# Optimization experiments

Hardware: AMD Instinct MI355X
Metric: run time of the kernel (lower is better)

Reference implementation:

```python
import jax, jax.numpy as jnp
import numpy as np

NH = 8            # num_heads
LN_EPS = 1e-5


def _alibi_slopes(n):
    # n is a power of two here (8)
    start = 2.0 ** (-2.0 ** (-(np.log2(n) - 3)))
    return np.array([start * (start ** i) for i in range(n)], dtype=np.float32)


def _ln(x, w, b):
    m = x.mean(-1, keepdims=True)
    v = ((x - m) ** 2).mean(-1, keepdims=True)
    return (x - m) / jnp.sqrt(v + LN_EPS) * w + b


def setup_inputs() -> dict:
    key = jax.random.key(0)
    B, S, D_in, H, L = 2, 2048, 192, 512, 4
    ks = jax.random.split(key, 8)
    p = lambda k, shape: 0.02 * jax.random.normal(k, shape, dtype=jnp.float32)
    return {
        "x": jax.random.normal(ks[0], (B, S, D_in), dtype=jnp.float32),
        "w_emb": p(ks[1], (H, D_in)), "b_emb": jnp.zeros((H,), jnp.float32),
        "ln1_w": jnp.ones((L, H), jnp.float32), "ln1_b": jnp.zeros((L, H), jnp.float32),
        "inp_w": p(ks[2], (L, 3 * H, H)), "inp_b": jnp.zeros((L, 3 * H), jnp.float32),
        "outp_w": p(ks[3], (L, H, H)), "outp_b": jnp.zeros((L, H), jnp.float32),
        "ln2_w": jnp.ones((L, H), jnp.float32), "ln2_b": jnp.zeros((L, H), jnp.float32),
        "w1": p(ks[4], (L, 4 * H, H)), "b1": jnp.zeros((L, 4 * H), jnp.float32),
        "w2": p(ks[5], (L, H, 4 * H)), "b2": jnp.zeros((L, H), jnp.float32),
        "fln_w": jnp.ones((H,), jnp.float32), "fln_b": jnp.zeros((H,), jnp.float32),
        "w_out": p(ks[6], (D_in, H)), "b_out": jnp.zeros((D_in,), jnp.float32),
    }


def reference(x, w_emb, b_emb, ln1_w, ln1_b, inp_w, inp_b, outp_w, outp_b,
              ln2_w, ln2_b, w1, b1, w2, b2, fln_w, fln_b, w_out, b_out):
    B, S, _ = x.shape
    H = w_emb.shape[0]
    L = ln1_w.shape[0]
    hd = H // NH
    scale = 1.0 / np.sqrt(hd)

    h = x @ w_emb.T + b_emb                                   # [B,S,H]

    # ALiBi + causal additive mask, shared across batch: [NH,S,S]
    slopes = jnp.asarray(_alibi_slopes(NH))
    pos = jnp.arange(S)
    rel = pos[:, None] - pos[None, :]                         # i - j
    causal = jnp.where(rel < 0, -jnp.inf, 0.0).astype(jnp.float32)
    mask = -slopes[:, None, None] * jnp.maximum(rel, 0).astype(jnp.float32) + causal

    for l in range(L):
        xn = _ln(h, ln1_w[l], ln1_b[l])
        qkv = xn @ inp_w[l].T + inp_b[l]                      # [B,S,3H]
        q, k, v = jnp.split(qkv, 3, axis=-1)
        q = q.reshape(B, S, NH, hd)
        k = k.reshape(B, S, NH, hd)
        v = v.reshape(B, S, NH, hd)
        scores = jnp.einsum('bqhd,bkhd->bhqk', q, k) * scale + mask[None]
        attn = jax.nn.softmax(scores, axis=-1)
        o = jnp.einsum('bhqk,bkhd->bqhd', attn, v).reshape(B, S, H)
        h = h + o @ outp_w[l].T + outp_b[l]
        xn2 = _ln(h, ln2_w[l], ln2_b[l])
        mlp = jax.nn.gelu(xn2 @ w1[l].T + b1[l], approximate=False) @ w2[l].T + b2[l]
        h = h + mlp

    h = _ln(h, fln_w, fln_b)
    return h @ w_out.T + b_out
```

## Files before the change

### kernel.cpp

```cpp
#include <hip/hip_runtime.h>
#include <hip/hip_bf16.h>
#include <math.h>

typedef short v8s __attribute__((ext_vector_type(8)));
typedef float v4f __attribute__((ext_vector_type(4)));
typedef unsigned int v2u __attribute__((ext_vector_type(2)));
typedef __hip_bfloat16 bf16;

#define LDQK 1056
#define LDVT 2080

__device__ inline short f2b(float f){
  __hip_bfloat16 h = __float2bfloat16(f);
  return __builtin_bit_cast(short, h);
}
__device__ inline unsigned int pack2t(float x, float y){
  unsigned int xb = __builtin_bit_cast(unsigned int, x);
  unsigned int yb = __builtin_bit_cast(unsigned int, y);
  return (xb >> 16) | (yb & 0xFFFF0000u);
}
__device__ inline v4f v4f_zero(){ v4f z = {0.f,0.f,0.f,0.f}; return z; }

__device__ inline void gload_lds16(const void* g, void* l){
  __builtin_amdgcn_global_load_lds(
      (__attribute__((address_space(1))) void*)(g),
      (__attribute__((address_space(3))) void*)(l), 16, 0, 0);
}

struct CvtSeg { const float* s; bf16* d; int n4; };
struct CvtArgs { CvtSeg seg[7]; };

__global__ __launch_bounds__(256) void k_cvt7(CvtArgs a){
  const CvtSeg sg = a.seg[blockIdx.y];
  int i = blockIdx.x*256 + threadIdx.x;
  const int stride = gridDim.x*256;
  for (; i < sg.n4; i += stride){
    float4 v = ((const float4*)sg.s)[i];
    short4 o;
    o.x = f2b(v.x); o.y = f2b(v.y); o.z = f2b(v.z); o.w = f2b(v.w);
    ((short4*)sg.d)[i] = o;
  }
}

__global__ __launch_bounds__(256) void k_ln(const float* __restrict__ x,
                                            const float* __restrict__ w,
                                            const float* __restrict__ b,
                                            bf16* __restrict__ out){
  const int row  = blockIdx.x*4 + (threadIdx.x>>6);
  const int lane = threadIdx.x & 63;
  const float* xr = x + (size_t)row*512 + lane*8;
  float4 a = *(const float4*)xr;
  float4 c = *(const float4*)(xr+4);
  float s  = a.x+a.y+a.z+a.w + c.x+c.y+c.z+c.w;
  float sq = a.x*a.x+a.y*a.y+a.z*a.z+a.w*a.w + c.x*c.x+c.y*c.y+c.z*c.z+c.w*c.w;
  #pragma unroll
  for (int m=1;m<64;m<<=1){ s += __shfl_xor(s,m); sq += __shfl_xor(sq,m); }
  const float mean = s*(1.f/512.f);
  const float rstd = rsqrtf(sq*(1.f/512.f) - mean*mean + 1e-5f);
  const float* wp = w + lane*8; const float* bp = b + lane*8;
  float4 w0 = *(const float4*)wp, w1v = *(const float4*)(wp+4);
  float4 b0 = *(const float4*)bp, b1v = *(const float4*)(bp+4);
  v8s o;
  o[0]=f2b((a.x-mean)*rstd*w0.x +b0.x);
  o[1]=f2b((a.y-mean)*rstd*w0.y +b0.y);
  o[2]=f2b((a.z-mean)*rstd*w0.z +b0.z);
  o[3]=f2b((a.w-mean)*rstd*w0.w +b0.w);
  o[4]=f2b((c.x-mean)*rstd*w1v.x+b1v.x);
  o[5]=f2b((c.y-mean)*rstd*w1v.y+b1v.y);
  o[6]=f2b((c.z-mean)*rstd*w1v.z+b1v.z);
  o[7]=f2b((c.w-mean)*rstd*w1v.w+b1v.w);
  *(v8s*)(out + (size_t)row*512 + lane*8) = o;
}

enum { EPI_F32=0, EPI_BF16=1, EPI_F32RES=2, EPI_GELU=3, EPI_VT=4, EPI_QKV=5 };

template<int BM, int BN, int BK, int WR, int EPI>
__global__ __launch_bounds__(256) void k_gemm(
    const bf16* __restrict__ A, const bf16* __restrict__ W,
    const float* __restrict__ bias,
    float* __restrict__ resf, bf16* __restrict__ outb,
    const int M, const int N, const int K, const int ldo)
{
  constexpr int WC = 4/WR;
  constexpr int FM = BM/(WR*16);
  constexpr int FN = BN/(WC*16);
  constexpr int KK = BK/32;
  constexpr int CPR = BK/8;
  __shared__ __align__(16) bf16 As[2][BM*BK];
  __shared__ __align__(16) bf16 Bs[2][BN*BK];
  const int tid  = threadIdx.x;
  const int wave = tid>>6, lane = tid&63;
  const int r = lane&15, g = lane>>4;
  const int bm = blockIdx.x*BM, bn = blockIdx.y*BN;
  const int wr = (WR==1) ? 0 : (wave>>1);
  const int wc = (WR==1) ? wave : (wave&1);

  v4f acc[FM][FN];
  #pragma unroll
  for (int i=0;i<FM;++i)
    #pragma unroll
    for (int j=0;j<FN;++j) acc[i][j] = v4f_zero();

  const int NT = K / BK;

  auto stage = [&](int buf, int kb){
    constexpr int ACH = BM*CPR;
    #pragma unroll
    for (int it=0; it<(ACH+255)/256; ++it){
      const int cb = it*256 + wave*64;
      if ((ACH & 255) == 0 || cb < ACH){
        const int cc = cb + lane;
        const bf16* gp = A + (size_t)(bm + cc/CPR)*K + kb + (cc%CPR)*8;
        gload_lds16(gp, &As[buf][cc*8]);
      }
    }
    constexpr int BCH = BN*CPR;
    #pragma unroll
    for (int it=0; it<(BCH+255)/256; ++it){
      const int cb = it*256 + wave*64;
      if ((BCH & 255) == 0 || cb < BCH){
        const int cc = cb + lane;
        const bf16* gp = W + (size_t)(bn + cc/CPR)*K + kb + (cc%CPR)*8;
        gload_lds16(gp, &Bs[buf][cc*8]);
      }
    }
  };

  stage(0, 0);
  int cur = 0;
  for (int t=0; t<NT; ++t){
    __syncthreads();
    if (t+1 < NT) stage(cur^1, (t+1)*BK);
    const bf16* ap = &As[cur][(wr*(BM/WR) + r)*BK + g*8];
    const bf16* bp = &Bs[cur][(wc*(BN/WC) + r)*BK + g*8];
    #pragma unroll
    for (int kk=0; kk<KK; ++kk){
      v8s af[FM], bfr[FN];
      #pragma unroll
      for (int i=0;i<FM;++i) af[i] = *(const v8s*)(ap + i*16*BK + kk*32);
      #pragma unroll
      for (int j=0;j<FN;++j) bfr[j] = *(const v8s*)(bp + j*16*BK + kk*32);
      #pragma unroll
      for (int i=0;i<FM;++i)
        #pragma unroll
        for (int j=0;j<FN;++j)
          acc[i][j] = __builtin_amdgcn_mfma_f32_16x16x32_bf16(af[i], bfr[j], acc[i][j], 0,0,0);
    }
    cur ^= 1;
  }

  #pragma unroll
  for (int j=0;j<FN;++j){
    const int col = bn + wc*(BN/WC) + j*16 + r;
    const float bv = bias[col];
    #pragma unroll
    for (int i=0;i<FM;++i){
      const int row0 = bm + wr*(BM/WR) + i*16 + g*4;
      if constexpr (EPI==EPI_QKV){
        if (col < 1024){
          #pragma unroll
          for (int q=0;q<4;++q)
            outb[(size_t)(row0+q)*LDQK + col] = __float2bfloat16(acc[i][j][q] + bv);
        } else {
          const int d = col - 1024;
          bf16* vt = (bf16*)resf
                   + (((size_t)(row0>>11)*8 + (d>>6))*64 + (d&63))*(size_t)LDVT + (row0&2047);
          short4 st;
          st.x = f2b(acc[i][j][0] + bv);
          st.y = f2b(acc[i][j][1] + bv);
          st.z = f2b(acc[i][j][2] + bv);
          st.w = f2b(acc[i][j][3] + bv);
          *(short4*)vt = st;
        }
      } else if constexpr (EPI==EPI_VT){
        bf16* vt = outb + (((size_t)(row0>>11)*8 + (col>>6))*64 + (col&63))*(size_t)ldo + (row0&2047);
        short4 st;
        st.x = f2b(acc[i][j][0] + bv);
        st.y = f2b(acc[i][j][1] + bv);
        st.z = f2b(acc[i][j][2] + bv);
        st.w = f2b(acc[i][j][3] + bv);
        *(short4*)vt = st;
      } else {
        #pragma unroll
        for (int q=0;q<4;++q){
          float v = acc[i][j][q] + bv;
          const size_t idx = (size_t)(row0+q)*ldo + col;
          if constexpr (EPI==EPI_F32)         resf[idx] = v;
          else if constexpr (EPI==EPI_F32RES) resf[idx] += v;
          else if constexpr (EPI==EPI_BF16)   outb[idx] = __float2bfloat16(v);
          else if constexpr (EPI==EPI_GELU){
            float gv = 0.5f*v*(1.f + erff(v*0.70710678118654752f));
            outb[idx] = __float2bfloat16(gv);
          }
        }
      }
    }
  }
}

__global__ __launch_bounds__(256) void k_attn(const bf16* __restrict__ qk,
                                              const bf16* __restrict__ vt,
                                              bf16* __restrict__ o){
  const int flat  = blockIdx.x;
  const int qi    = flat >> 4;
  const int head  = flat & 7;
  const int batch = (flat >> 3) & 1;
  const int sp = threadIdx.x>>6, lane = threadIdx.x&63;
  const int r = lane&15, g = lane>>4;
  const float LOG2E = 1.4426950408889634f;
  const float scale2 = 0.125f * LOG2E;
  const float slope2 = exp2f(-(float)(head+1)) * LOG2E;
  const bf16* qbase = qk + (size_t)batch*2048*LDQK + head*64;
  const bf16* kbase = qbase + 512;
  const bf16* vbase = vt + (size_t)(batch*8 + head)*64*LDVT;

  __shared__ float Ls[4][2][16];
  __shared__ __align__(16) v4f Os[4][4][64];
  __shared__ __align__(16) short Psw[4][16][40];

  const int w0 = qi, w1 = 127-qi;
  const int nt0 = (w0>>1) + 1;
  const int nt1 = (w1>>1) + 1;
  const int q0 = w0*16 + r, q1 = w1*16 + r;

  const bf16* q0p = qbase + (size_t)q0*LDQK + g*8;
  const bf16* q1p = qbase + (size_t)q1*LDQK + g*8;
  const v8s qf0A = *(const v8s*)q0p, qf0B = *(const v8s*)(q0p + 32);
  const v8s qf1A = *(const v8s*)q1p, qf1B = *(const v8s*)(q1p + 32);

  float cj[8];
  #pragma unroll
  for (int j=0;j<4;++j){ cj[j] = (float)j * slope2; cj[4+j] = (float)(16+j) * slope2; }

  v4f oacc0[4], oacc1[4];
  #pragma unroll
  for (int nf=0;nf<4;++nf){ oacc0[nf] = v4f_zero(); oacc1[nf] = v4f_zero(); }
  float l0 = 0.f, l1 = 0.f;

  v8s kf[4], kn[4], vf[4], vn[4];
  auto loadK = [&](v8s* d, const bf16* kp){
    d[0] = *(const v8s*)(kp);
    d[1] = *(const v8s*)(kp + 32);
    d[2] = *(const v8s*)(kp + (size_t)16*LDQK);
    d[3] = *(const v8s*)(kp + (size_t)16*LDQK + 32);
  };
  auto loadV = [&](v8s* d, const bf16* vp){
    #pragma unroll
    for (int nf=0;nf<4;++nf) d[nf] = *(const v8s*)(vp + (size_t)nf*16*LDVT);
  };

  auto processU = [&](const v8s& qfA, const v8s& qfB, int dd, bool last,
                      float& l, v4f* oa){
    v4f s0 = v4f_zero(), s1 = v4f_zero();
    __builtin_amdgcn_s_setprio(1);
    s0 = __builtin_amdgcn_mfma_f32_16x16x32_bf16(kf[0], qfA, s0, 0,0,0);
    s0 = __builtin_amdgcn_mfma_f32_16x16x32_bf16(kf[1], qfB, s0, 0,0,0);
    s1 = __builtin_amdgcn_mfma_f32_16x16x32_bf16(kf[2], qfA, s1, 0,0,0);
    s1 = __builtin_amdgcn_mfma_f32_16x16x32_bf16(kf[3], qfB, s1, 0,0,0);
    __builtin_amdgcn_s_setprio(0);
    const float base = (float)dd * slope2;
    float v[8];
    #pragma unroll
    for (int j=0;j<4;++j) v[j]   = fmaf(s0[j], scale2, base + cj[j]);
    #pragma unroll
    for (int j=0;j<4;++j) v[4+j] = fmaf(s1[j], scale2, base + cj[4+j]);
    if (last){
      #pragma unroll
      for (int j=0;j<4;++j){
        if (dd + j      > 0) v[j]   = -1e30f;
        if (dd + 16 + j > 0) v[4+j] = -1e30f;
      }
    }
    float p[8];
    #pragma unroll
    for (int j=0;j<8;++j){ p[j] = exp2f(v[j]); l += p[j]; }

    v2u lo; lo[0] = pack2t(p[0],p[1]); lo[1] = pack2t(p[2],p[3]);
    v2u hi; hi[0] = pack2t(p[4],p[5]); hi[1] = pack2t(p[6],p[7]);
    *(v2u*)&Psw[sp][r][g*4]      = lo;
    *(v2u*)&Psw[sp][r][16 + g*4] = hi;
    const v8s pf = *(const v8s*)&Psw[sp][r][g*8];

    __builtin_amdgcn_s_setprio(1);
    #pragma unroll
    for (int nf=0;nf<4;++nf)
      oa[nf] = __builtin_amdgcn_mfma_f32_16x16x32_bf16(vf[nf], pf, oa[nf], 0,0,0);
    __builtin_amdgcn_s_setprio(0);
  };

  const bf16* kp = kbase + (size_t)(sp*32 + r)*LDQK + g*8;
  const bf16* vp = vbase + (size_t)r*LDVT + sp*32 + g*8;
  int dd0 = sp*32 + g*4 - q0;
  int dd1 = sp*32 + g*4 - q1;

  loadK(kf, kp);
  loadV(vf, vp);
  for (int t = sp; t < nt1; t += 4){
    const bool more = (t+4 < nt1);
    if (more){
      loadK(kn, kp + (size_t)4*32*LDQK);
      loadV(vn, vp + 128);
    }

    processU(qf1A, qf1B, dd1, t == nt1-1, l1, oacc1);
    if (t < nt0)
      processU(qf0A, qf0B, dd0, t == nt0-1, l0, oacc0);

    if (more){
      #pragma unroll
      for (int i=0;i<4;++i){ kf[i] = kn[i]; vf[i] = vn[i]; }
      kp += (size_t)4*32*LDQK;
      vp += 128;
    }
    dd0 += 128; dd1 += 128;
  }

  l0 += __shfl_xor(l0, 16); l0 += __shfl_xor(l0, 32);
  l1 += __shfl_xor(l1, 16); l1 += __shfl_xor(l1, 32);

  if (g == 0){
    Ls[sp][0][r] = l0;
    Ls[sp][1][r] = l1;
  }

  auto merge = [&](int u, const int w){
    float L = 0.f;
    v4f O[4];
    #pragma unroll
    for (int nf=0;nf<4;++nf) O[nf] = v4f_zero();
    #pragma unroll
    for (int ss=0;ss<4;++ss){
      L += Ls[ss][u][r];
      #pragma unroll
      for (int nf=0;nf<4;++nf) O[nf] += Os[ss][nf][lane];
    }
    const float inv = 1.f/L;
    const int q = w*16 + r;
    bf16* orow = o + ((size_t)batch*2048 + q)*512 + head*64 + g*4;
    #pragma unroll
    for (int nf=0;nf<4;++nf){
      short4 st;
      st.x = f2b(O[nf][0]*inv);
      st.y = f2b(O[nf][1]*inv);
      st.z = f2b(O[nf][2]*inv);
      st.w = f2b(O[nf][3]*inv);
      *(short4*)(orow + nf*16) = st;
    }
  };

  #pragma unroll
  for (int nf=0;nf<4;++nf) Os[sp][nf][lane] = oacc0[nf];
  __syncthreads();
  if (sp == 0) merge(0, w0);
  __syncthreads();
  #pragma unroll
  for (int nf=0;nf<4;++nf) Os[sp][nf][lane] = oacc1[nf];
  __syncthreads();
  if (sp == 1) merge(1, w1);
}

extern "C" void kernel_launch(void* const* d_in, const int* in_sizes, int n_in,
                              void* d_out, int out_size, void* d_ws, size_t ws_size,
                              hipStream_t stream)
{
  const float* x     = (const float*)d_in[0];
  const float* w_emb = (const float*)d_in[1];
  const float* b_emb = (const float*)d_in[2];
  const float* ln1_w = (const float*)d_in[3];
  const float* ln1_b = (const float*)d_in[4];
  const float* inp_w = (const float*)d_in[5];
  const float* inp_b = (const float*)d_in[6];
  const float* outp_w= (const float*)d_in[7];
  const float* outp_b= (const float*)d_in[8];
  const float* ln2_w = (const float*)d_in[9];
  const float* ln2_b = (const float*)d_in[10];
  const float* w1    = (const float*)d_in[11];
  const float* b1    = (const float*)d_in[12];
  const float* w2    = (const float*)d_in[13];
  const float* b2    = (const float*)d_in[14];
  const float* fln_w = (const float*)d_in[15];
  const float* fln_b = (const float*)d_in[16];
  const float* w_out = (const float*)d_in[17];
  const float* b_out = (const float*)d_in[18];

  char* wsp = (char*)d_ws;
  auto alloc = [&](size_t bytes){ void* p = (void*)wsp; wsp += (bytes + 255) & ~(size_t)255; return p; };
  float* h     = (float*)alloc(4096UL*512*4);
  bf16* xn     = (bf16*) alloc(4096UL*512*2);
  bf16* qkb    = (bf16*) alloc(4096UL*LDQK*2);
  bf16* vtb    = (bf16*) alloc(2UL*8*64*LDVT*2);
  bf16* ob     = (bf16*) alloc(4096UL*512*2);
  bf16* a1     = (bf16*) alloc(4096UL*2048*2);
  bf16* xbf    = (bf16*) alloc(4096UL*192*2);
  bf16* wembB  = (bf16*) alloc(512UL*192*2);
  bf16* inpwB  = (bf16*) alloc(4UL*1536*512*2);
  bf16* outpwB = (bf16*) alloc(4UL*512*512*2);
  bf16* w1B    = (bf16*) alloc(4UL*2048*512*2);
  bf16* w2B    = (bf16*) alloc(4UL*512*2048*2);
  bf16* woutB  = (bf16*) alloc(192UL*512*2);

  CvtArgs ca;
  ca.seg[0] = { x,      xbf,    (int)(4096UL*192/4)      };
  ca.seg[1] = { w_emb,  wembB,  (int)(512UL*192/4)       };
  ca.seg[2] = { inp_w,  inpwB,  (int)(4UL*1536*512/4)    };
  ca.seg[3] = { outp_w, outpwB, (int)(4UL*512*512/4)     };
  ca.seg[4] = { w1,     w1B,    (int)(4UL*2048*512/4)    };
  ca.seg[5] = { w2,     w2B,    (int)(4UL*512*2048/4)    };
  ca.seg[6] = { w_out,  woutB,  (int)(192UL*512/4)       };
  k_cvt7<<<dim3(256,7), dim3(256), 0, stream>>>(ca);

  k_gemm<32,128,32,1, EPI_F32><<<dim3(128,4), 256, 0, stream>>>(
      xbf, wembB, b_emb, h, nullptr, 4096, 512, 192, 512);

  for (int l=0; l<4; ++l){
    k_ln<<<dim3(1024), dim3(256), 0, stream>>>(h, ln1_w + l*512, ln1_b + l*512, xn);
    k_gemm<64,128,64,2, EPI_QKV><<<dim3(64,12), 256, 0, stream>>>(
        xn, inpwB + (size_t)l*1536*512, inp_b + l*1536, (float*)vtb, qkb,
        4096, 1536, 512, LDQK);
    k_attn<<<dim3(1024), 256, 0, stream>>>(qkb, vtb, ob);
    k_gemm<32,128,64,1, EPI_F32RES><<<dim3(128,4), 256, 0, stream>>>(
        ob, outpwB + (size_t)l*512*512, outp_b + l*512, h, nullptr,
        4096, 512, 512, 512);
    k_ln<<<dim3(1024), dim3(256), 0, stream>>>(h, ln2_w + l*512, ln2_b + l*512, xn);
    k_gemm<128,128,64,2, EPI_GELU><<<dim3(32,16), 256, 0, stream>>>(
        xn, w1B + (size_t)l*2048*512, b1 + l*2048, nullptr, a1,
        4096, 2048, 512, 2048);
    k_gemm<32,128,64,1, EPI_F32RES><<<dim3(128,4), 256, 0, stream>>>(
        a1, w2B + (size_t)l*512*2048, b2 + l*512, h, nullptr,
        4096, 512, 2048, 512);
  }

  k_ln<<<dim3(1024), dim3(256), 0, stream>>>(h, fln_w, fln_b, xn);
  k_gemm<32,64,64,1, EPI_F32><<<dim3(128,3), 256, 0, stream>>>(
      xn, woutB, b_out, (float*)d_out, nullptr, 4096, 192, 512, 192);
}
```

Baseline: 534.9 us.

## Process four query tiles per attention block to reuse K/V loads

The attention kernel now handles four 16-row query tiles per block (qi, 63-qi, 64+qi, 127-qi) instead of two, and the grid shrinks from 1024 to 512 blocks. Each K/V fragment loaded from global memory feeds up to four query tiles, which roughly halves K/V read traffic. The pairing keeps per-block causal work balanced. In exchange, register pressure rises from the extra accumulators and Q fragments, fewer blocks are available to fill the GPU, and the merge step needs more block-wide synchronisation.

```diff
diff --git a/kernel.cpp b/kernel.cpp
--- a/kernel.cpp
+++ b/kernel.cpp
@@ -214,28 +214,34 @@
   const bf16* kbase = qbase + 512;
   const bf16* vbase = vt + (size_t)(batch*8 + head)*64*LDVT;
 
-  __shared__ float Ls[4][2][16];
+  __shared__ float Ls[4][4][16];
   __shared__ __align__(16) v4f Os[4][4][64];
   __shared__ __align__(16) short Psw[4][16][40];
 
-  const int w0 = qi, w1 = 127-qi;
-  const int nt0 = (w0>>1) + 1;
-  const int nt1 = (w1>>1) + 1;
-  const int q0 = w0*16 + r, q1 = w1*16 + r;
+  const int w0 = qi, w1 = 63-qi, w2 = 64+qi, w3 = 127-qi;
+  const int nt0 = (w0>>1)+1, nt1 = (w1>>1)+1, nt2 = (w2>>1)+1, nt3 = (w3>>1)+1;
+  const int q0 = w0*16 + r, q1 = w1*16 + r, q2 = w2*16 + r, q3 = w3*16 + r;
 
   const bf16* q0p = qbase + (size_t)q0*LDQK + g*8;
   const bf16* q1p = qbase + (size_t)q1*LDQK + g*8;
+  const bf16* q2p = qbase + (size_t)q2*LDQK + g*8;
+  const bf16* q3p = qbase + (size_t)q3*LDQK + g*8;
   const v8s qf0A = *(const v8s*)q0p, qf0B = *(const v8s*)(q0p + 32);
   const v8s qf1A = *(const v8s*)q1p, qf1B = *(const v8s*)(q1p + 32);
+  const v8s qf2A = *(const v8s*)q2p, qf2B = *(const v8s*)(q2p + 32);
+  const v8s qf3A = *(const v8s*)q3p, qf3B = *(const v8s*)(q3p + 32);
 
   float cj[8];
   #pragma unroll
   for (int j=0;j<4;++j){ cj[j] = (float)j * slope2; cj[4+j] = (float)(16+j) * slope2; }
 
-  v4f oacc0[4], oacc1[4];
-  #pragma unroll
-  for (int nf=0;nf<4;++nf){ oacc0[nf] = v4f_zero(); oacc1[nf] = v4f_zero(); }
-  float l0 = 0.f, l1 = 0.f;
+  v4f oacc0[4], oacc1[4], oacc2[4], oacc3[4];
+  #pragma unroll
+  for (int nf=0;nf<4;++nf){
+    oacc0[nf] = v4f_zero(); oacc1[nf] = v4f_zero();
+    oacc2[nf] = v4f_zero(); oacc3[nf] = v4f_zero();
+  }
+  float l0 = 0.f, l1 = 0.f, l2 = 0.f, l3 = 0.f;
 
   v8s kf[4], kn[4], vf[4], vn[4];
   auto loadK = [&](v8s* d, const bf16* kp){
@@ -292,19 +298,22 @@
   const bf16* vp = vbase + (size_t)r*LDVT + sp*32 + g*8;
   int dd0 = sp*32 + g*4 - q0;
   int dd1 = sp*32 + g*4 - q1;
+  int dd2 = sp*32 + g*4 - q2;
+  int dd3 = sp*32 + g*4 - q3;
 
   loadK(kf, kp);
   loadV(vf, vp);
-  for (int t = sp; t < nt1; t += 4){
-    const bool more = (t+4 < nt1);
+  for (int t = sp; t < nt3; t += 4){
+    const bool more = (t+4 < nt3);
     if (more){
       loadK(kn, kp + (size_t)4*32*LDQK);
       loadV(vn, vp + 128);
     }
 
-    processU(qf1A, qf1B, dd1, t == nt1-1, l1, oacc1);
-    if (t < nt0)
-      processU(qf0A, qf0B, dd0, t == nt0-1, l0, oacc0);
+    processU(qf3A, qf3B, dd3, t == nt3-1, l3, oacc3);
+    if (t < nt2) processU(qf2A, qf2B, dd2, t == nt2-1, l2, oacc2);
+    if (t < nt1) processU(qf1A, qf1B, dd1, t == nt1-1, l1, oacc1);
+    if (t < nt0) processU(qf0A, qf0B, dd0, t == nt0-1, l0, oacc0);
 
     if (more){
       #pragma unroll
@@ -312,15 +321,17 @@
       kp += (size_t)4*32*LDQK;
       vp += 128;
     }
-    dd0 += 128; dd1 += 128;
+    dd0 += 128; dd1 += 128; dd2 += 128; dd3 += 128;
   }
 
   l0 += __shfl_xor(l0, 16); l0 += __shfl_xor(l0, 32);
   l1 += __shfl_xor(l1, 16); l1 += __shfl_xor(l1, 32);
+  l2 += __shfl_xor(l2, 16); l2 += __shfl_xor(l2, 32);
+  l3 += __shfl_xor(l3, 16); l3 += __shfl_xor(l3, 32);
 
   if (g == 0){
-    Ls[sp][0][r] = l0;
-    Ls[sp][1][r] = l1;
+    Ls[sp][0][r] = l0; Ls[sp][1][r] = l1;
+    Ls[sp][2][r] = l2; Ls[sp][3][r] = l3;
   }
 
   auto merge = [&](int u, const int w){
@@ -357,6 +368,16 @@
   for (int nf=0;nf<4;++nf) Os[sp][nf][lane] = oacc1[nf];
   __syncthreads();
   if (sp == 1) merge(1, w1);
+  __syncthreads();
+  #pragma unroll
+  for (int nf=0;nf<4;++nf) Os[sp][nf][lane] = oacc2[nf];
+  __syncthreads();
+  if (sp == 2) merge(2, w2);
+  __syncthreads();
+  #pragma unroll
+  for (int nf=0;nf<4;++nf) Os[sp][nf][lane] = oacc3[nf];
+  __syncthreads();
+  if (sp == 3) merge(3, w3);
 }
 
 extern "C" void kernel_launch(void* const* d_in, const int* in_sizes, int n_in,
@@ -417,7 +438,7 @@
     k_gemm<64,128,64,2, EPI_QKV><<<dim3(64,12), 256, 0, stream>>>(
         xn, inpwB + (size_t)l*1536*512, inp_b + l*1536, (float*)vtb, qkb,
         4096, 1536, 512, LDQK);
-    k_attn<<<dim3(1024), 256, 0, stream>>>(qkb, vtb, ob);
+    k_attn<<<dim3(512), 256, 0, stream>>>(qkb, vtb, ob);
     k_gemm<32,128,64,1, EPI_F32RES><<<dim3(128,4), 256, 0, stream>>>(
         ob, outpwB + (size_t)l*512*512, outp_b + l*512, h, nullptr,
         4096, 512, 512, 512);
```

New measurement: 572.7 us. +7.1%, slower.
